# Kernel optimization log

Hardware: AMD Instinct MI355X
Metric: run time of the kernel (lower is better)

## Reference

```python
import jax, jax.numpy as jnp
from jax import lax
import numpy as np

B, CTX, TGT, D_MODEL = 2, 1024, 256, 512
EXPAND, D_STATE, D_CONV, N_LAYERS = 2, 16, 4, 2
D_INNER = EXPAND * D_MODEL
DT_RANK = (D_MODEL + 15) // 16  # 32, mamba_ssm default ceil(d_model/16)
LN_EPS = 1e-5


def setup_inputs() -> dict:
    key = jax.random.key(0)
    ks = jax.random.split(key, 20)
    s = 0.02
    inp = {
        "context_repr": jax.random.normal(ks[0], (B, CTX, D_MODEL), jnp.float32),
        "target_time_emb": jax.random.normal(ks[1], (B, TGT, D_MODEL), jnp.float32),
        "target_var_emb": jax.random.normal(ks[2], (B, TGT, D_MODEL), jnp.float32),
        "target_count": TGT,
        # position_proj / output_proj / LayerNorm params
        "pos_w": jax.random.normal(ks[3], (D_MODEL, 2 * D_MODEL), jnp.float32) * s,
        "pos_b": jnp.zeros((D_MODEL,), jnp.float32),
        "outp_w": jax.random.normal(ks[4], (D_MODEL, D_MODEL), jnp.float32) * s,
        "outp_b": jnp.zeros((D_MODEL,), jnp.float32),
        "ln_g": jnp.ones((D_MODEL,), jnp.float32),
        "ln_b": jnp.zeros((D_MODEL,), jnp.float32),
        # stacked per-layer Mamba params
        "in_w": jax.random.normal(ks[5], (N_LAYERS, 2 * D_INNER, D_MODEL), jnp.float32) * s,
        "conv_w": jax.random.normal(ks[6], (N_LAYERS, D_INNER, D_CONV), jnp.float32) * s,
        "conv_b": jnp.zeros((N_LAYERS, D_INNER), jnp.float32),
        "xproj_w": jax.random.normal(ks[7], (N_LAYERS, DT_RANK + 2 * D_STATE, D_INNER), jnp.float32) * s,
        "dt_w": jax.random.normal(ks[8], (N_LAYERS, D_INNER, DT_RANK), jnp.float32) * s,
        "dt_b": jax.random.normal(ks[9], (N_LAYERS, D_INNER), jnp.float32) * s,
        # A_log init as in mamba_ssm: A = arange(1, d_state+1) repeated over d_inner
        "A_log": jnp.broadcast_to(
            jnp.log(jnp.arange(1, D_STATE + 1, dtype=jnp.float32)),
            (N_LAYERS, D_INNER, D_STATE),
        ).copy(),
        "D_skip": jnp.ones((N_LAYERS, D_INNER), jnp.float32),
        "out_w": jax.random.normal(ks[10], (N_LAYERS, D_MODEL, D_INNER), jnp.float32) * s,
    }
    return inp


def _mamba_block(x, in_w, conv_w, conv_b, xproj_w, dt_w, dt_b, A_log, D_skip, out_w):
    # x: [B, L, d_model]
    Bb, L, _ = x.shape
    xz = jnp.einsum("bld,ed->ble", x, in_w)          # [B, L, 2*d_inner]
    xc, z = jnp.split(xz, 2, axis=-1)
    # causal depthwise conv1d (Conv1d pad=d_conv-1 then [..., :L])
    xt = xc.transpose(0, 2, 1)                        # [B, d_inner, L]
    conv = lax.conv_general_dilated(
        xt, conv_w[:, None, :], (1,), [(D_CONV - 1, 0)],
        feature_group_count=D_INNER,
        dimension_numbers=("NCH", "OIH", "NCH"),
    )
    u = jax.nn.silu(conv + conv_b[None, :, None]).transpose(0, 2, 1)  # [B, L, d_inner]
    x_dbl = jnp.einsum("bld,ed->ble", u, xproj_w)     # [B, L, dt_rank + 2*d_state]
    dt, Bm, Cm = jnp.split(x_dbl, [DT_RANK, DT_RANK + D_STATE], axis=-1)
    delta = jax.nn.softplus(jnp.einsum("blr,dr->bld", dt, dt_w) + dt_b)  # [B, L, d_inner]
    A = -jnp.exp(A_log)                               # [d_inner, d_state]
    dA = jnp.exp(delta[..., None] * A)                # [B, L, d_inner, d_state]
    dBu = delta[..., None] * Bm[:, :, None, :] * u[..., None]

    def step(h, inps):
        dA_t, dBu_t, C_t = inps                       # [B,d_inner,d_state], same, [B,d_state]
        h = dA_t * h + dBu_t
        y = jnp.einsum("bds,bs->bd", h, C_t)
        return h, y

    h0 = jnp.zeros((Bb, D_INNER, D_STATE), x.dtype)
    _, ys = lax.scan(step, h0, (dA.transpose(1, 0, 2, 3), dBu.transpose(1, 0, 2, 3), Cm.transpose(1, 0, 2)))
    y = ys.transpose(1, 0, 2) + u * D_skip            # [B, L, d_inner]
    y = y * jax.nn.silu(z)
    return jnp.einsum("ble,de->bld", y, out_w)        # [B, L, d_model]


def reference(context_repr, target_time_emb, target_var_emb, target_count,
              pos_w, pos_b, outp_w, outp_b, ln_g, ln_b,
              in_w, conv_w, conv_b, xproj_w, dt_w, dt_b, A_log, D_skip, out_w):
    tc = jnp.concatenate([target_time_emb, target_var_emb], axis=-1)      # [B, T, 2*d]
    pos = jnp.einsum("blk,dk->bld", tc, pos_w) + pos_b                    # [B, T, d]
    x = jnp.concatenate([context_repr, pos], axis=1)                      # [B, C+T, d]
    for i in range(N_LAYERS):
        x = x + _mamba_block(x, in_w[i], conv_w[i], conv_b[i], xproj_w[i],
                             dt_w[i], dt_b[i], A_log[i], D_skip[i], out_w[i])
    mu = jnp.mean(x, axis=-1, keepdims=True)
    var = jnp.mean(jnp.square(x - mu), axis=-1, keepdims=True)
    x = (x - mu) * lax.rsqrt(var + LN_EPS) * ln_g + ln_b
    tgt = x[:, -int(target_count):]
    return jnp.einsum("bld,ed->ble", tgt, outp_w) + outp_b
```

## Files before the change

kernel.cpp:

```cpp
#include <hip/hip_runtime.h>
#include <hip/hip_bf16.h>

#define B_     2
#define CTX_   1024
#define TGT_   256
#define DM_    512
#define L_     1280
#define DI_    1024
#define DS_    16
#define DCONV_ 4
#define NL_    2
#define DTR_   32
#define MROWS_ (B_*L_)
#define NC_    40
#define CL_    32
#define XDBL_N_ (MROWS_*64)

typedef unsigned short u16;
typedef __attribute__((ext_vector_type(8))) __bf16 bf16x8;
typedef __attribute__((ext_vector_type(4))) float f32x4;

__device__ __forceinline__ float sigmoidf_(float v){ return 1.f/(1.f+__expf(-v)); }
__device__ __forceinline__ float siluf_(float v){ return v*sigmoidf_(v); }
__device__ __forceinline__ float softplusf_(float v){ return (v>20.f)?v:log1pf(__expf(v)); }
__device__ __forceinline__ u16 f2b(float f){
    union { float f; unsigned u; } x; x.f = f;
    unsigned u = x.u;
    return (u16)((u + 0x7fffu + ((u>>16)&1u)) >> 16);
}
__device__ __forceinline__ float b2f(u16 v){ return __uint_as_float(((unsigned)v)<<16); }
__device__ __forceinline__ void gload_lds16(const void* g, void* l){
    __builtin_amdgcn_global_load_lds((const __attribute__((address_space(1))) unsigned*)g,
                                     (__attribute__((address_space(3))) unsigned*)l, 16, 0, 0);
}
#define PIPE_SYNC do{ asm volatile("s_waitcnt vmcnt(0)" ::: "memory"); \
                      __builtin_amdgcn_sched_barrier(0); \
                      __builtin_amdgcn_s_barrier(); \
                      __builtin_amdgcn_sched_barrier(0); }while(0)

#define G0_ 262144
#define G1_ 131072
#define G2_  65536
#define G3_  32768
#define G4_  16384
__global__ __launch_bounds__(256) void k_init(const float* __restrict__ s0, const float* __restrict__ s1,
                                              const float* __restrict__ s2, const float* __restrict__ s3,
                                              const float* __restrict__ s4,
                                              u16* d0, u16* d1, u16* d2, u16* d3, u16* d4,
                                              const float* __restrict__ ctx, const float* __restrict__ te,
                                              const float* __restrict__ ve, float* __restrict__ x,
                                              u16* __restrict__ xb, u16* __restrict__ tcb){
    int blk = blockIdx.x;
    if (blk < 1984){
        int g = blk*256 + threadIdx.x;
        const float* s; u16* d; int base;
        if      (g < G0_)                { s=s0; d=d0; base=g*8; }
        else if (g < G0_+G1_)            { s=s1; d=d1; base=(g-G0_)*8; }
        else if (g < G0_+G1_+G2_)        { s=s2; d=d2; base=(g-G0_-G1_)*8; }
        else if (g < G0_+G1_+G2_+G3_)    { s=s3; d=d3; base=(g-G0_-G1_-G2_)*8; }
        else                             { s=s4; d=d4; base=(g-G0_-G1_-G2_-G3_)*8; }
        float4 a = *(const float4*)&s[base];
        float4 b = *(const float4*)&s[base+4];
        union { u16 us[8]; uint4 v; } o;
        o.us[0]=f2b(a.x); o.us[1]=f2b(a.y); o.us[2]=f2b(a.z); o.us[3]=f2b(a.w);
        o.us[4]=f2b(b.x); o.us[5]=f2b(b.y); o.us[6]=f2b(b.z); o.us[7]=f2b(b.w);
        *(uint4*)&d[base] = o.v;
    } else if (blk < 1984+1024){
        int e = ((blk-1984)*256 + threadIdx.x)*4;
        int d = e % DM_;
        int l = (e/DM_) % CTX_;
        int b = e/(DM_*CTX_);
        float4 v = *(const float4*)&ctx[e];
        size_t o = ((size_t)(b*L_+l))*DM_ + d;
        *(float4*)&x[o] = v;
        union { u16 us[4]; uint2 q; } p;
        p.us[0]=f2b(v.x); p.us[1]=f2b(v.y); p.us[2]=f2b(v.z); p.us[3]=f2b(v.w);
        *(uint2*)&xb[o] = p.q;
    } else {
        int e = ((blk-1984-1024)*256 + threadIdx.x)*4;
        int k = e % (2*DM_);
        int r = e / (2*DM_);
        float4 v = (k < DM_) ? *(const float4*)&te[(size_t)r*DM_ + k]
                             : *(const float4*)&ve[(size_t)r*DM_ + (k-DM_)];
        union { u16 us[4]; uint2 q; } p;
        p.us[0]=f2b(v.x); p.us[1]=f2b(v.y); p.us[2]=f2b(v.z); p.us[3]=f2b(v.w);
        *(uint2*)&tcb[e] = p.q;
    }
}

__global__ __launch_bounds__(256) void k_conv_silu(const u16* __restrict__ xzb, const float* __restrict__ cw,
                                                   const float* __restrict__ cb, u16* __restrict__ ub){
    int e = (blockIdx.x*256 + threadIdx.x)*4;
    int d = e % DI_;
    int l = (e/DI_) % L_;
    int b = e/(DI_*L_);
    const u16* base = xzb + (size_t)b*L_*2048 + d;
    float4 w0 = *(const float4*)&cw[(d+0)*4];
    float4 w1 = *(const float4*)&cw[(d+1)*4];
    float4 w2 = *(const float4*)&cw[(d+2)*4];
    float4 w3 = *(const float4*)&cw[(d+3)*4];
    float4 bb = *(const float4*)&cb[d];
    float a0=bb.x, a1=bb.y, a2=bb.z, a3=bb.w;
    #pragma unroll
    for (int k=0;k<DCONV_;++k){
        int ll = l-3+k;
        if (ll >= 0){
            uint2 q = *(const uint2*)&base[(size_t)ll*2048];
            float x0=b2f((u16)(q.x&0xffffu)), x1=b2f((u16)(q.x>>16));
            float x2=b2f((u16)(q.y&0xffffu)), x3=b2f((u16)(q.y>>16));
            float c0 = (k==0)?w0.x:(k==1)?w0.y:(k==2)?w0.z:w0.w;
            float c1 = (k==0)?w1.x:(k==1)?w1.y:(k==2)?w1.z:w1.w;
            float c2 = (k==0)?w2.x:(k==1)?w2.y:(k==2)?w2.z:w2.w;
            float c3 = (k==0)?w3.x:(k==1)?w3.y:(k==2)?w3.z:w3.w;
            a0=fmaf(x0,c0,a0); a1=fmaf(x1,c1,a1); a2=fmaf(x2,c2,a2); a3=fmaf(x3,c3,a3);
        }
    }
    union { u16 us[4]; uint2 q; } o;
    o.us[0]=f2b(siluf_(a0)); o.us[1]=f2b(siluf_(a1));
    o.us[2]=f2b(siluf_(a2)); o.us[3]=f2b(siluf_(a3));
    *(uint2*)&ub[e] = o.q;
}

template<bool WB>
__global__ __launch_bounds__(256) void k_mmx(const u16* __restrict__ A, int lda,
                                             const u16* __restrict__ Bw, int ldb,
                                             float* __restrict__ C, int ldc,
                                             const float* __restrict__ bias, int K,
                                             u16* __restrict__ Cb, int ldcb){
    __shared__ u16 As[2][128*32];
    __shared__ u16 Bs[2][128*32];
    int tid = threadIdx.x;
    int wave = tid >> 6, lane = tid & 63;
    int bm = blockIdx.y*128, bn = blockIdx.x*128;
    int wr = (wave>>1)*64, wc = (wave&1)*64;
    f32x4 acc[4][4] = {};
    int lrow = lane & 15, lk = (lane>>4)*8;
    int dphys0 = wave*1024 + lane*16;
    int dphys1 = dphys0 + 4096;
    int alog0  = dphys0 ^ (((dphys0>>7)&7)<<4);
    int alog1  = dphys1 ^ (((dphys1>>7)&7)<<4);
    int grow0  = alog0 >> 6,        grow1  = alog1 >> 6;
    int gcol0  = (alog0 & 63) >> 1, gcol1  = (alog1 & 63) >> 1;
    const u16* Ar0 = A  + (size_t)(bm+grow0)*lda + gcol0;
    const u16* Ar1 = A  + (size_t)(bm+grow1)*lda + gcol1;
    const u16* Br0 = Bw + (size_t)(bn+grow0)*ldb + gcol0;
    const u16* Br1 = Bw + (size_t)(bn+grow1)*ldb + gcol1;
    int aoff[4], boff[4];
    #pragma unroll
    for (int f=0; f<4; ++f){
        int ra = wr + f*16 + lrow, rb = wc + f*16 + lrow;
        aoff[f] = (ra*64 + lk*2) ^ (((ra>>1)&7)<<4);
        boff[f] = (rb*64 + lk*2) ^ (((rb>>1)&7)<<4);
    }
    int nt = K >> 5;
    auto stage = [&](int t, int buf){
        int k0 = t*32;
        gload_lds16(Ar0 + k0, &As[buf][wave*512]);
        gload_lds16(Ar1 + k0, &As[buf][2048 + wave*512]);
        gload_lds16(Br0 + k0, &Bs[buf][wave*512]);
        gload_lds16(Br1 + k0, &Bs[buf][2048 + wave*512]);
    };
    stage(0, 0);
    PIPE_SYNC;
    int cur = 0;
    for (int t=0; t<nt; ++t){
        if (t+1 < nt) stage(t+1, cur^1);
        bf16x8 af[4], bfr[4];
        #pragma unroll
        for (int f=0; f<4; ++f){
            af [f] = *(const bf16x8*)((const char*)As[cur] + aoff[f]);
            bfr[f] = *(const bf16x8*)((const char*)Bs[cur] + boff[f]);
        }
        #pragma unroll
        for (int fm=0; fm<4; ++fm)
            #pragma unroll
            for (int fn=0; fn<4; ++fn)
                acc[fm][fn] = __builtin_amdgcn_mfma_f32_16x16x32_bf16(af[fm], bfr[fn], acc[fm][fn], 0,0,0);
        PIPE_SYNC;
        cur ^= 1;
    }
    #pragma unroll
    for (int fm=0; fm<4; ++fm){
        int m0 = bm + wr + fm*16 + (lane>>4)*4;
        #pragma unroll
        for (int fn=0; fn<4; ++fn){
            int n = bn + wc + fn*16 + (lane&15);
            float bsv = (!WB && bias) ? bias[n] : 0.f;
            #pragma unroll
            for (int j=0; j<4; ++j){
                float v = acc[fm][fn][j] + bsv;
                if (WB) Cb[(size_t)(m0+j)*ldcb + n] = f2b(v);
                else    C [(size_t)(m0+j)*ldc  + n] = v;
            }
        }
    }
}

template<bool ACC, bool SPLIT, bool SCAT>
__global__ __launch_bounds__(256) void k_mmx64(const u16* __restrict__ A, int lda,
                                               const u16* __restrict__ Bw, int ldb,
                                               float* __restrict__ C, int ldc,
                                               const float* __restrict__ bias, int ksteps,
                                               u16* __restrict__ Cb, int ldcb, int splitStride){
    __shared__ u16 As[2][64*32];
    __shared__ u16 Bs[2][64*32];
    int tid = threadIdx.x;
    int wave = tid >> 6, lane = tid & 63;
    int bm = blockIdx.y*64;
    int bn    = SPLIT ? 0 : blockIdx.x*64;
    int kbase = SPLIT ? blockIdx.x*ksteps*32 : 0;
    int wr = (wave>>1)*32, wc = (wave&1)*32;
    f32x4 acc[2][2] = {};
    int lrow = lane & 15, lk = (lane>>4)*8;
    int dphys = wave*1024 + lane*16;
    int alog  = dphys ^ (((dphys>>7)&7)<<4);
    int grow  = alog >> 6;
    int gcol  = (alog & 63) >> 1;
    const u16* Ar = A  + (size_t)(bm+grow)*lda + gcol;
    const u16* Br = Bw + (size_t)(bn+grow)*ldb + gcol;
    int aoff[2], boff[2];
    #pragma unroll
    for (int f=0; f<2; ++f){
        int ra = wr + f*16 + lrow, rb = wc + f*16 + lrow;
        aoff[f] = (ra*64 + lk*2) ^ (((ra>>1)&7)<<4);
        boff[f] = (rb*64 + lk*2) ^ (((rb>>1)&7)<<4);
    }
    auto stage = [&](int t, int buf){
        int k0 = kbase + t*32;
        gload_lds16(Ar + k0, &As[buf][wave*512]);
        gload_lds16(Br + k0, &Bs[buf][wave*512]);
    };
    stage(0, 0);
    PIPE_SYNC;
    int cur = 0;
    for (int t = 0; t < ksteps; ++t){
        if (t+1 < ksteps) stage(t+1, cur^1);
        bf16x8 af[2], bfr[2];
        #pragma unroll
        for (int f=0; f<2; ++f){
            af [f] = *(const bf16x8*)((const char*)As[cur] + aoff[f]);
            bfr[f] = *(const bf16x8*)((const char*)Bs[cur] + boff[f]);
        }
        #pragma unroll
        for (int fm=0; fm<2; ++fm)
            #pragma unroll
            for (int fn=0; fn<2; ++fn)
                acc[fm][fn] = __builtin_amdgcn_mfma_f32_16x16x32_bf16(af[fm], bfr[fn], acc[fm][fn], 0,0,0);
        PIPE_SYNC;
        cur ^= 1;
    }
    float* Cout = SPLIT ? (C + (size_t)blockIdx.x*splitStride) : C;
    #pragma unroll
    for (int fm=0; fm<2; ++fm){
        int m0 = bm + wr + fm*16 + (lane>>4)*4;
        #pragma unroll
        for (int fn=0; fn<2; ++fn){
            int n = bn + wc + fn*16 + (lane&15);
            float bsv = (!SPLIT && bias) ? bias[n] : 0.f;
            #pragma unroll
            for (int j=0; j<4; ++j){
                float v = acc[fm][fn][j] + bsv;
                int m = m0 + j;
                if (SCAT){
                    int xrow = (m>>8)*L_ + CTX_ + (m&255);
                    C [(size_t)xrow*ldc  + n] = v;
                    Cb[(size_t)xrow*ldcb + n] = f2b(v);
                } else {
                    size_t off = (size_t)m*ldc + n;
                    if (ACC) v += Cout[off];
                    Cout[off] = v;
                    if (!SPLIT && Cb) Cb[(size_t)m*ldcb + n] = f2b(v);
                }
            }
        }
    }
}

__global__ __launch_bounds__(256) void k_red8(const float* __restrict__ part, float* __restrict__ out){
    int j = (blockIdx.x*256 + threadIdx.x)*4;
    float4 s = *(const float4*)&part[j];
    #pragma unroll
    for (int p=1;p<8;++p){
        float4 t = *(const float4*)&part[(size_t)p*XDBL_N_ + j];
        s.x+=t.x; s.y+=t.y; s.z+=t.z; s.w+=t.w;
    }
    *(float4*)&out[j] = s;
}

__global__ __launch_bounds__(256) void k_scan1(const u16* __restrict__ ub, const float* __restrict__ xdbl,
                                               const float* __restrict__ dtw, const float* __restrict__ dtb,
                                               const float* __restrict__ Alog,
                                               float* __restrict__ hend, float* __restrict__ P){
    __shared__ float sX[CL_*64];
    __shared__ float sW[64*33];
    __shared__ float sDtb[64];
    __shared__ float sDel[CL_*64];
    __shared__ u16   sU[CL_*64];
    int blk = blockIdx.x;
    int dgrp = blk & 15;
    int c = (blk>>4) % NC_;
    int b = blk/(16*NC_);
    int d0 = dgrp*64;
    int tid = threadIdx.x;
    size_t rowbase = (size_t)(b*L_ + c*CL_);
    #pragma unroll
    for (int j=0;j<2;++j){
        int e = tid*4 + j*1024;
        *(float4*)&sX[e] = *(const float4*)&xdbl[rowbase*64 + e];
        int st=e>>6, dd=e&63;
        *(uint2*)&sU[e] = *(const uint2*)&ub[(rowbase+st)*DI_ + d0 + dd];
    }
    {
        int w0 = tid*8, dr = w0>>5, kk = w0&31;
        float4 wa = *(const float4*)&dtw[(size_t)(d0+dr)*DTR_ + kk];
        float4 wb = *(const float4*)&dtw[(size_t)(d0+dr)*DTR_ + kk + 4];
        sW[dr*33+kk+0]=wa.x; sW[dr*33+kk+1]=wa.y; sW[dr*33+kk+2]=wa.z; sW[dr*33+kk+3]=wa.w;
        sW[dr*33+kk+4]=wb.x; sW[dr*33+kk+5]=wb.y; sW[dr*33+kk+6]=wb.z; sW[dr*33+kk+7]=wb.w;
        if (tid < 64) sDtb[tid] = dtb[d0+tid];
    }
    __syncthreads();
    #pragma unroll
    for (int i=0;i<8;++i){
        int idx = tid + i*256;
        int t = idx>>6, dd = idx&63;
        float acc = sDtb[dd];
        #pragma unroll
        for (int k=0;k<DTR_;++k) acc = fmaf(sX[t*64+k], sW[dd*33+k], acc);
        sDel[idx] = softplusf_(acc);
    }
    __syncthreads();
    int dl = tid>>2, sg = (tid&3)*4;
    int d = d0 + dl;
    float A[4];
    #pragma unroll
    for (int i=0;i<4;++i) A[i] = -__expf(Alog[d*DS_ + sg + i]);
    float h[4] = {0,0,0,0}, Pl[4] = {1.f,1.f,1.f,1.f};
    #pragma unroll
    for (int t=0;t<CL_;++t){
        float delta = sDel[t*64+dl];
        float uu    = b2f(sU[t*64+dl]);
        float du    = delta*uu;
        #pragma unroll
        for (int i=0;i<4;++i){
            float a = __expf(delta*A[i]);
            h[i]  = fmaf(a, h[i], du*sX[t*64 + 32 + sg + i]);
            Pl[i] *= a;
        }
    }
    size_t ob = ((size_t)((b*NC_+c)*DI_) + d)*DS_ + sg;
    *(float4*)&hend[ob] = make_float4(h[0],h[1],h[2],h[3]);
    *(float4*)&P[ob]    = make_float4(Pl[0],Pl[1],Pl[2],Pl[3]);
}

__global__ __launch_bounds__(256) void k_scan2(float* __restrict__ hend, const float* __restrict__ P){
    int g = blockIdx.x*256 + threadIdx.x;
    int s = g & 15;
    int d = (g>>4) & 1023;
    int b = g>>14;
    size_t base = ((size_t)b*NC_*DI_ + d)*DS_ + s;
    const size_t cs = (size_t)DI_*DS_;
    float h = 0.f;
    for (int c0=0;c0<NC_;c0+=8){
        float he[8], p[8];
        #pragma unroll
        for (int j=0;j<8;++j){ size_t idx = base + (size_t)(c0+j)*cs; he[j]=hend[idx]; p[j]=P[idx]; }
        #pragma unroll
        for (int j=0;j<8;++j){ size_t idx = base + (size_t)(c0+j)*cs; hend[idx]=h; h=fmaf(p[j],h,he[j]); }
    }
}

__global__ __launch_bounds__(256) void k_scan3(const u16* __restrict__ ub, const float* __restrict__ xdbl,
                                               const float* __restrict__ dtw, const float* __restrict__ dtb,
                                               const u16* __restrict__ xzb,
                                               const float* __restrict__ Alog, const float* __restrict__ Dsk,
                                               const float* __restrict__ hstart, u16* __restrict__ yb){
    __shared__ float sX[CL_*64];
    __shared__ float sW[64*33];
    __shared__ float sDtb[64];
    __shared__ float sDel[CL_*64];
    __shared__ u16   sU[CL_*64];
    __shared__ float sY[CL_*64];
    int blk = blockIdx.x;
    int dgrp = blk & 15;
    int c = (blk>>4) % NC_;
    int b = blk/(16*NC_);
    int d0 = dgrp*64;
    int tid = threadIdx.x;
    size_t rowbase = (size_t)(b*L_ + c*CL_);
    #pragma unroll
    for (int j=0;j<2;++j){
        int e = tid*4 + j*1024;
        *(float4*)&sX[e] = *(const float4*)&xdbl[rowbase*64 + e];
        int st=e>>6, dd=e&63;
        *(uint2*)&sU[e] = *(const uint2*)&ub[(rowbase+st)*DI_ + d0 + dd];
    }
    {
        int w0 = tid*8, dr = w0>>5, kk = w0&31;
        float4 wa = *(const float4*)&dtw[(size_t)(d0+dr)*DTR_ + kk];
        float4 wb = *(const float4*)&dtw[(size_t)(d0+dr)*DTR_ + kk + 4];
        sW[dr*33+kk+0]=wa.x; sW[dr*33+kk+1]=wa.y; sW[dr*33+kk+2]=wa.z; sW[dr*33+kk+3]=wa.w;
        sW[dr*33+kk+4]=wb.x; sW[dr*33+kk+5]=wb.y; sW[dr*33+kk+6]=wb.z; sW[dr*33+kk+7]=wb.w;
        if (tid < 64) sDtb[tid] = dtb[d0+tid];
    }
    __syncthreads();
    #pragma unroll
    for (int i=0;i<8;++i){
        int idx = tid + i*256;
        int t = idx>>6, dd = idx&63;
        float acc = sDtb[dd];
        #pragma unroll
        for (int k=0;k<DTR_;++k) acc = fmaf(sX[t*64+k], sW[dd*33+k], acc);
        sDel[idx] = softplusf_(acc);
    }
    __syncthreads();
    int dl = tid>>2, sg = (tid&3)*4;
    int d = d0 + dl;
    float A[4];
    #pragma unroll
    for (int i=0;i<4;++i) A[i] = -__expf(Alog[d*DS_ + sg + i]);
    size_t ib = ((size_t)((b*NC_+c)*DI_) + d)*DS_ + sg;
    float4 h4 = *(const float4*)&hstart[ib];
    float h[4] = {h4.x, h4.y, h4.z, h4.w};
    #pragma unroll
    for (int t=0;t<CL_;++t){
        float delta = sDel[t*64+dl];
        float uu    = b2f(sU[t*64+dl]);
        float du    = delta*uu;
        float yt = 0.f;
        #pragma unroll
        for (int i=0;i<4;++i){
            float a = __expf(delta*A[i]);
            h[i] = fmaf(a, h[i], du*sX[t*64 + 32 + sg + i]);
            yt   = fmaf(h[i], sX[t*64 + 48 + sg + i], yt);
        }
        yt += __shfl_xor(yt, 1);
        yt += __shfl_xor(yt, 2);
        if ((tid&3)==0) sY[t*64+dl] = yt;
    }
    __syncthreads();
    #pragma unroll
    for (int j=0;j<2;++j){
        int e = tid*4 + j*1024, st = e>>6, dd = e&63;
        size_t off = (rowbase+st)*DI_ + d0 + dd;
        float4 dskv = *(const float4*)&Dsk[d0+dd];
        uint2 zz = *(const uint2*)&xzb[(rowbase+st)*2048 + DI_ + d0 + dd];
        float z0 = __uint_as_float(zz.x<<16),  z1 = __uint_as_float(zz.x & 0xffff0000u);
        float z2 = __uint_as_float(zz.y<<16),  z3 = __uint_as_float(zz.y & 0xffff0000u);
        float u0 = b2f(sU[e+0]), u1 = b2f(sU[e+1]), u2 = b2f(sU[e+2]), u3 = b2f(sU[e+3]);
        union { u16 us[4]; uint2 q; } o;
        o.us[0] = f2b((sY[e+0] + u0*dskv.x) * siluf_(z0));
        o.us[1] = f2b((sY[e+1] + u1*dskv.y) * siluf_(z1));
        o.us[2] = f2b((sY[e+2] + u2*dskv.z) * siluf_(z2));
        o.us[3] = f2b((sY[e+3] + u3*dskv.w) * siluf_(z3));
        *(uint2*)&yb[off] = o.q;
    }
}

__global__ __launch_bounds__(256) void k_ln_tgt(const float* __restrict__ x, const float* __restrict__ g_,
                                                const float* __restrict__ b_, u16* __restrict__ xnb){
    int r = blockIdx.x;
    int b = r / TGT_, t = r % TGT_;
    const float* row = x + ((size_t)(b*L_+CTX_+t))*DM_;
    int tid = threadIdx.x;
    float2 v = *(const float2*)&row[tid*2];
    float s = v.x+v.y, sq = v.x*v.x+v.y*v.y;
    #pragma unroll
    for (int off=32; off; off>>=1){ s += __shfl_down(s,off); sq += __shfl_down(sq,off); }
    __shared__ float ss[4], ssq[4];
    int w = tid>>6, ln = tid&63;
    if (ln==0){ ss[w]=s; ssq[w]=sq; }
    __syncthreads();
    if (tid==0){
        float S=ss[0]+ss[1]+ss[2]+ss[3], Q=ssq[0]+ssq[1]+ssq[2]+ssq[3];
        float mu = S/(float)DM_;
        float var = Q/(float)DM_ - mu*mu;
        ss[0]=mu; ssq[0]=rsqrtf(var+1e-5f);
    }
    __syncthreads();
    float mu=ss[0], rs=ssq[0];
    xnb[(size_t)r*DM_ + tid*2+0] = f2b((v.x-mu)*rs*g_[tid*2+0] + b_[tid*2+0]);
    xnb[(size_t)r*DM_ + tid*2+1] = f2b((v.y-mu)*rs*g_[tid*2+1] + b_[tid*2+1]);
}

extern "C" void kernel_launch(void* const* d_in, const int* in_sizes, int n_in,
                              void* d_out, int out_size, void* d_ws, size_t ws_size,
                              hipStream_t stream) {
    const float* ctx    = (const float*)d_in[0];
    const float* te     = (const float*)d_in[1];
    const float* ve     = (const float*)d_in[2];
    const float* pos_w  = (const float*)d_in[4];
    const float* pos_b  = (const float*)d_in[5];
    const float* outp_w = (const float*)d_in[6];
    const float* outp_b = (const float*)d_in[7];
    const float* ln_g   = (const float*)d_in[8];
    const float* ln_b   = (const float*)d_in[9];
    const float* in_w   = (const float*)d_in[10];
    const float* conv_w = (const float*)d_in[11];
    const float* conv_b = (const float*)d_in[12];
    const float* xproj_w= (const float*)d_in[13];
    const float* dt_w   = (const float*)d_in[14];
    const float* dt_b   = (const float*)d_in[15];
    const float* A_log  = (const float*)d_in[16];
    const float* D_skip = (const float*)d_in[17];
    const float* out_w  = (const float*)d_in[18];
    float* out = (float*)d_out;

    float* ws    = (float*)d_ws;
    float* x     = ws;
    float* xdbl  = x     + 1310720;
    float* hend  = xdbl  + 163840;
    float* P     = hend  + 1310720;
    float* xdblp = P     + 1310720;
    u16*  xb    = (u16*)(xdblp + 1310720);
    u16*  tcb   = xb    + 1310720;
    u16*  yb    = tcb   + 524288;
    u16*  xnb   = yb    + 2621440;
    u16*  ub    = xnb   + 262144;
    u16*  xzb   = ub    + 2621440;
    u16*  inwb  = xzb   + 5242880;
    u16*  outwb = inwb  + 2097152;
    u16*  poswb = outwb + 1048576;
    u16*  outpwb= poswb + 524288;
    u16*  xpwb  = outpwb+ 262144;

    k_init<<<3520, 256, 0, stream>>>(in_w, out_w, pos_w, outp_w, xproj_w,
                                     inwb, outwb, poswb, outpwb, xpwb,
                                     ctx, te, ve, x, xb, tcb);
    k_mmx64<false,false,true><<<dim3(8,8), 256, 0, stream>>>(tcb, 2*DM_, poswb, 2*DM_, x, DM_, pos_b, 32, xb, DM_, 0);

    for (int i=0;i<NL_;++i){
        const u16*   inwbi  = inwb + (size_t)i*2*DI_*DM_;
        const float* cw     = conv_w  + (size_t)i*DI_*DCONV_;
        const float* cb     = conv_b  + (size_t)i*DI_;
        const u16*   xpwbi  = xpwb + (size_t)i*(DTR_+2*DS_)*DI_;
        const float* dtw    = dt_w    + (size_t)i*DI_*DTR_;
        const float* dtb    = dt_b    + (size_t)i*DI_;
        const float* Ai     = A_log   + (size_t)i*DI_*DS_;
        const float* Dsk    = D_skip  + (size_t)i*DI_;
        const u16*   outwbi = outwb + (size_t)i*DM_*DI_;

        k_mmx<true><<<dim3(16,20), 256, 0, stream>>>(xb, DM_, inwbi, DM_, nullptr, 0, nullptr, DM_, xzb, 2*DI_);
        k_conv_silu<<<2560, 256, 0, stream>>>(xzb, cw, cb, ub);
        k_mmx64<false,true,false><<<dim3(8,40), 256, 0, stream>>>(ub, DI_, xpwbi, DI_, xdblp, 64, nullptr, 4, nullptr, 0, XDBL_N_);
        k_red8<<<160, 256, 0, stream>>>(xdblp, xdbl);
        k_scan1<<<1280, 256, 0, stream>>>(ub, xdbl, dtw, dtb, Ai, hend, P);
        k_scan2<<<128, 256, 0, stream>>>(hend, P);
        k_scan3<<<1280, 256, 0, stream>>>(ub, xdbl, dtw, dtb, xzb, Ai, Dsk, hend, yb);
        k_mmx64<true,false,false><<<dim3(8,40), 256, 0, stream>>>(yb, DI_, outwbi, DI_, x, DM_, nullptr, 32, xb, DM_, 0);
    }

    k_ln_tgt<<<512, 256, 0, stream>>>(x, ln_g, ln_b, xnb);
    k_mmx64<false,false,false><<<dim3(8,8), 256, 0, stream>>>(xnb, DM_, outpwb, DM_, out, DM_, outp_b, 16, nullptr, 0, 0);
}
```

Measured before the change: 250.2 us.

## Use 8-wave GEMM blocks, halve scan chunk length, fuse split-K reduction into scans

The GEMM kernels move from 4 to 8 waves per block, so each wave owns a smaller output tile. In the 64-tile kernel, half the waves stage A and the other half stage B. The scan now uses 80 chunks of 16 steps instead of 40 of 32, which doubles the number of blocks in scan1 and scan3. The separate k_red8 kernel is removed, and the scans sum the 8 split-K partials directly. This saves a launch and a round trip to memory, but the reduction is now done twice, once in each scan. Smaller tiles per wave also lower MFMA work per LDS load, and scan2 must now combine more chunks.

Measured after the change: 238.2 us. 4.8% less time.

```diff
diff --git a/kernel.cpp b/kernel.cpp
--- a/kernel.cpp
+++ b/kernel.cpp
@@ -12,8 +12,8 @@
 #define NL_    2
 #define DTR_   32
 #define MROWS_ (B_*L_)
-#define NC_    40
-#define CL_    32
+#define NC_    80
+#define CL_    16
 #define XDBL_N_ (MROWS_*64)
 
 typedef unsigned short u16;
@@ -122,7 +122,7 @@
 }
 
 template<bool WB>
-__global__ __launch_bounds__(256) void k_mmx(const u16* __restrict__ A, int lda,
+__global__ __launch_bounds__(512) void k_mmx(const u16* __restrict__ A, int lda,
                                              const u16* __restrict__ Bw, int ldb,
                                              float* __restrict__ C, int ldc,
                                              const float* __restrict__ bias, int K,
@@ -132,49 +132,46 @@
     int tid = threadIdx.x;
     int wave = tid >> 6, lane = tid & 63;
     int bm = blockIdx.y*128, bn = blockIdx.x*128;
-    int wr = (wave>>1)*64, wc = (wave&1)*64;
-    f32x4 acc[4][4] = {};
+    int wr = (wave>>2)*64, wc = (wave&3)*32;
+    f32x4 acc[4][2] = {};
     int lrow = lane & 15, lk = (lane>>4)*8;
-    int dphys0 = wave*1024 + lane*16;
-    int dphys1 = dphys0 + 4096;
-    int alog0  = dphys0 ^ (((dphys0>>7)&7)<<4);
-    int alog1  = dphys1 ^ (((dphys1>>7)&7)<<4);
-    int grow0  = alog0 >> 6,        grow1  = alog1 >> 6;
-    int gcol0  = (alog0 & 63) >> 1, gcol1  = (alog1 & 63) >> 1;
-    const u16* Ar0 = A  + (size_t)(bm+grow0)*lda + gcol0;
-    const u16* Ar1 = A  + (size_t)(bm+grow1)*lda + gcol1;
-    const u16* Br0 = Bw + (size_t)(bn+grow0)*ldb + gcol0;
-    const u16* Br1 = Bw + (size_t)(bn+grow1)*ldb + gcol1;
-    int aoff[4], boff[4];
+    int dphys = tid*16;
+    int alog  = dphys ^ (((dphys>>7)&7)<<4);
+    int grow  = alog >> 6;
+    int gcol  = (alog & 63) >> 1;
+    const u16* Ar = A  + (size_t)(bm+grow)*lda + gcol;
+    const u16* Br = Bw + (size_t)(bn+grow)*ldb + gcol;
+    int aoff[4], boff[2];
     #pragma unroll
     for (int f=0; f<4; ++f){
-        int ra = wr + f*16 + lrow, rb = wc + f*16 + lrow;
+        int ra = wr + f*16 + lrow;
         aoff[f] = (ra*64 + lk*2) ^ (((ra>>1)&7)<<4);
+    }
+    #pragma unroll
+    for (int f=0; f<2; ++f){
+        int rb = wc + f*16 + lrow;
         boff[f] = (rb*64 + lk*2) ^ (((rb>>1)&7)<<4);
     }
     int nt = K >> 5;
     auto stage = [&](int t, int buf){
         int k0 = t*32;
-        gload_lds16(Ar0 + k0, &As[buf][wave*512]);
-        gload_lds16(Ar1 + k0, &As[buf][2048 + wave*512]);
-        gload_lds16(Br0 + k0, &Bs[buf][wave*512]);
-        gload_lds16(Br1 + k0, &Bs[buf][2048 + wave*512]);
+        gload_lds16(Ar + k0, &As[buf][wave*512]);
+        gload_lds16(Br + k0, &Bs[buf][wave*512]);
     };
     stage(0, 0);
     PIPE_SYNC;
     int cur = 0;
     for (int t=0; t<nt; ++t){
         if (t+1 < nt) stage(t+1, cur^1);
-        bf16x8 af[4], bfr[4];
-        #pragma unroll
-        for (int f=0; f<4; ++f){
-            af [f] = *(const bf16x8*)((const char*)As[cur] + aoff[f]);
-            bfr[f] = *(const bf16x8*)((const char*)Bs[cur] + boff[f]);
-        }
+        bf16x8 af[4], bfr[2];
+        #pragma unroll
+        for (int f=0; f<4; ++f) af[f]  = *(const bf16x8*)((const char*)As[cur] + aoff[f]);
+        #pragma unroll
+        for (int f=0; f<2; ++f) bfr[f] = *(const bf16x8*)((const char*)Bs[cur] + boff[f]);
         #pragma unroll
         for (int fm=0; fm<4; ++fm)
             #pragma unroll
-            for (int fn=0; fn<4; ++fn)
+            for (int fn=0; fn<2; ++fn)
                 acc[fm][fn] = __builtin_amdgcn_mfma_f32_16x16x32_bf16(af[fm], bfr[fn], acc[fm][fn], 0,0,0);
         PIPE_SYNC;
         cur ^= 1;
@@ -183,7 +180,7 @@
     for (int fm=0; fm<4; ++fm){
         int m0 = bm + wr + fm*16 + (lane>>4)*4;
         #pragma unroll
-        for (int fn=0; fn<4; ++fn){
+        for (int fn=0; fn<2; ++fn){
             int n = bn + wc + fn*16 + (lane&15);
             float bsv = (!WB && bias) ? bias[n] : 0.f;
             #pragma unroll
@@ -197,7 +194,7 @@
 }
 
 template<bool ACC, bool SPLIT, bool SCAT>
-__global__ __launch_bounds__(256) void k_mmx64(const u16* __restrict__ A, int lda,
+__global__ __launch_bounds__(512) void k_mmx64(const u16* __restrict__ A, int lda,
                                                const u16* __restrict__ Bw, int ldb,
                                                float* __restrict__ C, int ldc,
                                                const float* __restrict__ bias, int ksteps,
@@ -209,43 +206,41 @@
     int bm = blockIdx.y*64;
     int bn    = SPLIT ? 0 : blockIdx.x*64;
     int kbase = SPLIT ? blockIdx.x*ksteps*32 : 0;
-    int wr = (wave>>1)*32, wc = (wave&1)*32;
-    f32x4 acc[2][2] = {};
+    int wr = (wave>>2)*32, wc = (wave&3)*16;
+    f32x4 acc[2] = {};
     int lrow = lane & 15, lk = (lane>>4)*8;
-    int dphys = wave*1024 + lane*16;
+    int w4 = wave & 3;
+    int dphys = w4*1024 + lane*16;
     int alog  = dphys ^ (((dphys>>7)&7)<<4);
     int grow  = alog >> 6;
     int gcol  = (alog & 63) >> 1;
-    const u16* Ar = A  + (size_t)(bm+grow)*lda + gcol;
-    const u16* Br = Bw + (size_t)(bn+grow)*ldb + gcol;
-    int aoff[2], boff[2];
+    bool isB = wave >= 4;
+    const u16* Sr = isB ? (Bw + (size_t)(bn+grow)*ldb + gcol)
+                        : (A  + (size_t)(bm+grow)*lda + gcol);
+    u16* dst0 = isB ? &Bs[0][w4*512] : &As[0][w4*512];
+    u16* dst1 = isB ? &Bs[1][w4*512] : &As[1][w4*512];
+    int aoff[2], boff;
     #pragma unroll
     for (int f=0; f<2; ++f){
-        int ra = wr + f*16 + lrow, rb = wc + f*16 + lrow;
+        int ra = wr + f*16 + lrow;
         aoff[f] = (ra*64 + lk*2) ^ (((ra>>1)&7)<<4);
-        boff[f] = (rb*64 + lk*2) ^ (((rb>>1)&7)<<4);
-    }
+    }
+    { int rb = wc + lrow; boff = (rb*64 + lk*2) ^ (((rb>>1)&7)<<4); }
     auto stage = [&](int t, int buf){
-        int k0 = kbase + t*32;
-        gload_lds16(Ar + k0, &As[buf][wave*512]);
-        gload_lds16(Br + k0, &Bs[buf][wave*512]);
+        gload_lds16(Sr + kbase + t*32, buf ? dst1 : dst0);
     };
     stage(0, 0);
     PIPE_SYNC;
     int cur = 0;
     for (int t = 0; t < ksteps; ++t){
         if (t+1 < ksteps) stage(t+1, cur^1);
-        bf16x8 af[2], bfr[2];
-        #pragma unroll
-        for (int f=0; f<2; ++f){
-            af [f] = *(const bf16x8*)((const char*)As[cur] + aoff[f]);
-            bfr[f] = *(const bf16x8*)((const char*)Bs[cur] + boff[f]);
-        }
+        bf16x8 af[2], bfr;
+        #pragma unroll
+        for (int f=0; f<2; ++f) af[f] = *(const bf16x8*)((const char*)As[cur] + aoff[f]);
+        bfr = *(const bf16x8*)((const char*)Bs[cur] + boff);
         #pragma unroll
         for (int fm=0; fm<2; ++fm)
-            #pragma unroll
-            for (int fn=0; fn<2; ++fn)
-                acc[fm][fn] = __builtin_amdgcn_mfma_f32_16x16x32_bf16(af[fm], bfr[fn], acc[fm][fn], 0,0,0);
+            acc[fm] = __builtin_amdgcn_mfma_f32_16x16x32_bf16(af[fm], bfr, acc[fm], 0,0,0);
         PIPE_SYNC;
         cur ^= 1;
     }
@@ -253,41 +248,27 @@
     #pragma unroll
     for (int fm=0; fm<2; ++fm){
         int m0 = bm + wr + fm*16 + (lane>>4)*4;
-        #pragma unroll
-        for (int fn=0; fn<2; ++fn){
-            int n = bn + wc + fn*16 + (lane&15);
-            float bsv = (!SPLIT && bias) ? bias[n] : 0.f;
-            #pragma unroll
-            for (int j=0; j<4; ++j){
-                float v = acc[fm][fn][j] + bsv;
-                int m = m0 + j;
-                if (SCAT){
-                    int xrow = (m>>8)*L_ + CTX_ + (m&255);
-                    C [(size_t)xrow*ldc  + n] = v;
-                    Cb[(size_t)xrow*ldcb + n] = f2b(v);
-                } else {
-                    size_t off = (size_t)m*ldc + n;
-                    if (ACC) v += Cout[off];
-                    Cout[off] = v;
-                    if (!SPLIT && Cb) Cb[(size_t)m*ldcb + n] = f2b(v);
-                }
+        int n = bn + wc + (lane&15);
+        float bsv = (!SPLIT && bias) ? bias[n] : 0.f;
+        #pragma unroll
+        for (int j=0; j<4; ++j){
+            float v = acc[fm][j] + bsv;
+            int m = m0 + j;
+            if (SCAT){
+                int xrow = (m>>8)*L_ + CTX_ + (m&255);
+                C [(size_t)xrow*ldc  + n] = v;
+                Cb[(size_t)xrow*ldcb + n] = f2b(v);
+            } else {
+                size_t off = (size_t)m*ldc + n;
+                if (ACC) v += Cout[off];
+                Cout[off] = v;
+                if (!SPLIT && Cb) Cb[(size_t)m*ldcb + n] = f2b(v);
             }
         }
     }
 }
 
-__global__ __launch_bounds__(256) void k_red8(const float* __restrict__ part, float* __restrict__ out){
-    int j = (blockIdx.x*256 + threadIdx.x)*4;
-    float4 s = *(const float4*)&part[j];
-    #pragma unroll
-    for (int p=1;p<8;++p){
-        float4 t = *(const float4*)&part[(size_t)p*XDBL_N_ + j];
-        s.x+=t.x; s.y+=t.y; s.z+=t.z; s.w+=t.w;
-    }
-    *(float4*)&out[j] = s;
-}
-
-__global__ __launch_bounds__(256) void k_scan1(const u16* __restrict__ ub, const float* __restrict__ xdbl,
+__global__ __launch_bounds__(256) void k_scan1(const u16* __restrict__ ub, const float* __restrict__ xdblp,
                                                const float* __restrict__ dtw, const float* __restrict__ dtb,
                                                const float* __restrict__ Alog,
                                                float* __restrict__ hend, float* __restrict__ P){
@@ -303,14 +284,17 @@
     int d0 = dgrp*64;
     int tid = threadIdx.x;
     size_t rowbase = (size_t)(b*L_ + c*CL_);
-    #pragma unroll
-    for (int j=0;j<2;++j){
-        int e = tid*4 + j*1024;
-        *(float4*)&sX[e] = *(const float4*)&xdbl[rowbase*64 + e];
+    {
+        int e = tid*4;
+        float4 s4 = *(const float4*)&xdblp[rowbase*64 + e];
+        #pragma unroll
+        for (int p=1;p<8;++p){
+            float4 t4 = *(const float4*)&xdblp[(size_t)p*XDBL_N_ + rowbase*64 + e];
+            s4.x+=t4.x; s4.y+=t4.y; s4.z+=t4.z; s4.w+=t4.w;
+        }
+        *(float4*)&sX[e] = s4;
         int st=e>>6, dd=e&63;
         *(uint2*)&sU[e] = *(const uint2*)&ub[(rowbase+st)*DI_ + d0 + dd];
-    }
-    {
         int w0 = tid*8, dr = w0>>5, kk = w0&31;
         float4 wa = *(const float4*)&dtw[(size_t)(d0+dr)*DTR_ + kk];
         float4 wb = *(const float4*)&dtw[(size_t)(d0+dr)*DTR_ + kk + 4];
@@ -320,7 +304,7 @@
     }
     __syncthreads();
     #pragma unroll
-    for (int i=0;i<8;++i){
+    for (int i=0;i<4;++i){
         int idx = tid + i*256;
         int t = idx>>6, dd = idx&63;
         float acc = sDtb[dd];
@@ -369,7 +353,7 @@
     }
 }
 
-__global__ __launch_bounds__(256) void k_scan3(const u16* __restrict__ ub, const float* __restrict__ xdbl,
+__global__ __launch_bounds__(256) void k_scan3(const u16* __restrict__ ub, const float* __restrict__ xdblp,
                                                const float* __restrict__ dtw, const float* __restrict__ dtb,
                                                const u16* __restrict__ xzb,
                                                const float* __restrict__ Alog, const float* __restrict__ Dsk,
@@ -387,14 +371,17 @@
     int d0 = dgrp*64;
     int tid = threadIdx.x;
     size_t rowbase = (size_t)(b*L_ + c*CL_);
-    #pragma unroll
-    for (int j=0;j<2;++j){
-        int e = tid*4 + j*1024;
-        *(float4*)&sX[e] = *(const float4*)&xdbl[rowbase*64 + e];
+    {
+        int e = tid*4;
+        float4 s4 = *(const float4*)&xdblp[rowbase*64 + e];
+        #pragma unroll
+        for (int p=1;p<8;++p){
+            float4 t4 = *(const float4*)&xdblp[(size_t)p*XDBL_N_ + rowbase*64 + e];
+            s4.x+=t4.x; s4.y+=t4.y; s4.z+=t4.z; s4.w+=t4.w;
+        }
+        *(float4*)&sX[e] = s4;
         int st=e>>6, dd=e&63;
         *(uint2*)&sU[e] = *(const uint2*)&ub[(rowbase+st)*DI_ + d0 + dd];
-    }
-    {
         int w0 = tid*8, dr = w0>>5, kk = w0&31;
         float4 wa = *(const float4*)&dtw[(size_t)(d0+dr)*DTR_ + kk];
         float4 wb = *(const float4*)&dtw[(size_t)(d0+dr)*DTR_ + kk + 4];
@@ -404,7 +391,7 @@
     }
     __syncthreads();
     #pragma unroll
-    for (int i=0;i<8;++i){
+    for (int i=0;i<4;++i){
         int idx = tid + i*256;
         int t = idx>>6, dd = idx&63;
         float acc = sDtb[dd];
@@ -438,9 +425,8 @@
         if ((tid&3)==0) sY[t*64+dl] = yt;
     }
     __syncthreads();
-    #pragma unroll
-    for (int j=0;j<2;++j){
-        int e = tid*4 + j*1024, st = e>>6, dd = e&63;
+    {
+        int e = tid*4, st = e>>6, dd = e&63;
         size_t off = (rowbase+st)*DI_ + d0 + dd;
         float4 dskv = *(const float4*)&Dsk[d0+dd];
         uint2 zz = *(const uint2*)&xzb[(rowbase+st)*2048 + DI_ + d0 + dd];
@@ -507,10 +493,9 @@
 
     float* ws    = (float*)d_ws;
     float* x     = ws;
-    float* xdbl  = x     + 1310720;
-    float* hend  = xdbl  + 163840;
-    float* P     = hend  + 1310720;
-    float* xdblp = P     + 1310720;
+    float* hend  = x     + 1310720;
+    float* P     = hend  + 2621440;
+    float* xdblp = P     + 2621440;
     u16*  xb    = (u16*)(xdblp + 1310720);
     u16*  tcb   = xb    + 1310720;
     u16*  yb    = tcb   + 524288;
@@ -526,7 +511,7 @@
     k_init<<<3520, 256, 0, stream>>>(in_w, out_w, pos_w, outp_w, xproj_w,
                                      inwb, outwb, poswb, outpwb, xpwb,
                                      ctx, te, ve, x, xb, tcb);
-    k_mmx64<false,false,true><<<dim3(8,8), 256, 0, stream>>>(tcb, 2*DM_, poswb, 2*DM_, x, DM_, pos_b, 32, xb, DM_, 0);
+    k_mmx64<false,false,true><<<dim3(8,8), 512, 0, stream>>>(tcb, 2*DM_, poswb, 2*DM_, x, DM_, pos_b, 32, xb, DM_, 0);
 
     for (int i=0;i<NL_;++i){
         const u16*   inwbi  = inwb + (size_t)i*2*DI_*DM_;
@@ -539,16 +524,15 @@
         const float* Dsk    = D_skip  + (size_t)i*DI_;
         const u16*   outwbi = outwb + (size_t)i*DM_*DI_;
 
-        k_mmx<true><<<dim3(16,20), 256, 0, stream>>>(xb, DM_, inwbi, DM_, nullptr, 0, nullptr, DM_, xzb, 2*DI_);
+        k_mmx<true><<<dim3(16,20), 512, 0, stream>>>(xb, DM_, inwbi, DM_, nullptr, 0, nullptr, DM_, xzb, 2*DI_);
         k_conv_silu<<<2560, 256, 0, stream>>>(xzb, cw, cb, ub);
-        k_mmx64<false,true,false><<<dim3(8,40), 256, 0, stream>>>(ub, DI_, xpwbi, DI_, xdblp, 64, nullptr, 4, nullptr, 0, XDBL_N_);
-        k_red8<<<160, 256, 0, stream>>>(xdblp, xdbl);
-        k_scan1<<<1280, 256, 0, stream>>>(ub, xdbl, dtw, dtb, Ai, hend, P);
+        k_mmx64<false,true,false><<<dim3(8,40), 512, 0, stream>>>(ub, DI_, xpwbi, DI_, xdblp, 64, nullptr, 4, nullptr, 0, XDBL_N_);
+        k_scan1<<<2560, 256, 0, stream>>>(ub, xdblp, dtw, dtb, Ai, hend, P);
         k_scan2<<<128, 256, 0, stream>>>(hend, P);
-        k_scan3<<<1280, 256, 0, stream>>>(ub, xdbl, dtw, dtb, xzb, Ai, Dsk, hend, yb);
-        k_mmx64<true,false,false><<<dim3(8,40), 256, 0, stream>>>(yb, DI_, outwbi, DI_, x, DM_, nullptr, 32, xb, DM_, 0);
+        k_scan3<<<2560, 256, 0, stream>>>(ub, xdblp, dtw, dtb, xzb, Ai, Dsk, hend, yb);
+        k_mmx64<true,false,false><<<dim3(8,40), 512, 0, stream>>>(yb, DI_, outwbi, DI_, x, DM_, nullptr, 32, xb, DM_, 0);
     }
 
     k_ln_tgt<<<512, 256, 0, stream>>>(x, ln_g, ln_b, xnb);
-    k_mmx64<false,false,false><<<dim3(8,8), 256, 0, stream>>>(xnb, DM_, outpwb, DM_, out, DM_, outp_b, 16, nullptr, 0, 0);
-}
+    k_mmx64<false,false,false><<<dim3(8,8), 512, 0, stream>>>(xnb, DM_, outpwb, DM_, out, DM_, outp_b, 16, nullptr, 0, 0);
+}
```
